# Kernel tuning notes

Hardware: AMD Instinct MI355X
Metric: run time of the kernel (lower is better)

The kernel has to match this reference:

```python
import jax, jax.numpy as jnp
import numpy as np

L, KV, H, D, DM, F, V = 6, 1, 4, 256, 1152, 6912, 65536
HIST, T = 4095, 1
EPS = 1e-6


def setup_inputs():
    key = jax.random.key(0)
    ks = jax.random.split(key, 24)
    n = lambda k, s, sc=0.02: jax.random.normal(k, s, dtype=jnp.float32) * sc
    sf = D ** -0.25  # head_dim^-0.25 baked into q/k norm weights as in the source
    return {
        "input_ids": jax.random.randint(ks[0], (1, T), 0, V, dtype=jnp.int32),
        "attn_flag": 0,  # decode step: additive causal mask zeroed, as in the repo
        "key_cache": n(ks[1], (L, KV, D, HIST), 0.5),
        "value_cache": n(ks[2], (L, KV, HIST, D), 0.5),
        "embed_table": jax.random.randint(ks[3], (V, DM), 0, 256, dtype=jnp.int32),
        "embed_scale": jax.random.uniform(ks[4], (V, 1), minval=1e-4, maxval=1e-2, dtype=jnp.float32),
        "embed_zp": -jax.random.uniform(ks[5], (V, 1), minval=0.0, maxval=0.5, dtype=jnp.float32),
        "w_in_ln": 1.0 + n(ks[6], (L, DM)),
        "w_q_norm": (1.0 + n(ks[7], (L, D))) * sf,
        "w_k_norm": (1.0 + n(ks[8], (L, D))) * sf,
        "Wq": n(ks[9], (L, DM, H * D)),
        "Wk": n(ks[10], (L, DM, KV * D)),
        "Wv": n(ks[11], (L, DM, KV * D)),
        "Wo": n(ks[12], (L, H * D, DM)),
        "w_post_attn_ln": 1.0 + n(ks[13], (L, DM)),
        "w_pre_ffn_ln": 1.0 + n(ks[14], (L, DM)),
        "w_post_ffn_ln": 1.0 + n(ks[15], (L, DM)),
        "Wg": n(ks[16], (L, DM, F)),
        "Wu": n(ks[17], (L, DM, F)),
        "Wd": n(ks[18], (L, F, DM)),
        "w_final_norm": 1.0 + n(ks[19], (DM,)),
        "W_lm": n(ks[20], (DM, V)),
        "is_sliding": (jnp.arange(L) % 6) != 5,  # 5 local : 1 global pattern
    }


def _rms(x, w):
    return w * x / jnp.sqrt(jnp.mean(x * x, axis=-1, keepdims=True) + EPS)


def _rot_half(x, axis):
    x1, x2 = jnp.split(x, 2, axis=axis)
    return jnp.concatenate([-x2, x1], axis=axis)


def _rope(base, hist, S, d):
    pos = jnp.arange(hist, S, dtype=jnp.float32)[:, None]
    theta = base ** (-(jnp.arange(0, d, 2, dtype=jnp.float32) / d))
    ang = pos * theta
    c = jnp.concatenate([jnp.cos(ang)] * 2, axis=-1).astype(jnp.float16).astype(jnp.float32)
    s = jnp.concatenate([jnp.sin(ang)] * 2, axis=-1).astype(jnp.float16).astype(jnp.float32)
    return c, s  # (T, D), half-precision roundtrip mimics the .half() tables


def reference(input_ids, attn_flag, key_cache, value_cache, embed_table, embed_scale,
              embed_zp, w_in_ln, w_q_norm, w_k_norm, Wq, Wk, Wv, Wo, w_post_attn_ln,
              w_pre_ffn_ln, w_post_ffn_ln, Wg, Wu, Wd, w_final_norm, W_lm, is_sliding):
    Lc, KVc, Dd, hist = key_cache.shape
    Tq = input_ids.shape[1]
    S = hist + Tq
    Hh = Wq.shape[-1] // Dd
    G = Hh // KVc
    cos_g, sin_g = _rope(10000.0, hist, S, Dd)    # assigned to 'global' exactly as in source
    cos_l, sin_l = _rope(1000000.0, hist, S, Dd)  # assigned to 'local'
    mask = (jnp.arange(S)[None, :] > jnp.arange(Tq)[:, None]).astype(jnp.float32) * (-128.0 * float(attn_flag))  # (T,S)
    # int8-dequant embedding lookup: uint8 codes * per-row scale + per-row zero point
    h = embed_table[input_ids].astype(jnp.float32) * embed_scale[input_ids] + embed_zp[input_ids]  # (1,T,DM)

    def body(h, xs):
        ck, cv, slide, w_in, w_qn, w_kn, wq, wk, wv, wo, w_pa, w_pf, w_pof, wg, wu, wd = xs
        cq = jnp.where(slide, cos_l, cos_g)
        sq = jnp.where(slide, sin_l, sin_g)
        ckk, skk = cq.T, sq.T  # (D,T) for keys
        resid = h
        hn = _rms(h, w_in)                                                  # (1,T,DM)
        q = _rms((hn @ wq).reshape(Tq, Hh, Dd), w_qn).transpose(1, 0, 2)    # (H,T,D)
        k = _rms((hn @ wk).reshape(Tq, KVc, Dd), w_kn).transpose(1, 2, 0)   # (KV,D,T)
        v = (hn @ wv).reshape(Tq, KVc, Dd).transpose(1, 0, 2)               # (KV,T,D)
        q = q * cq + _rot_half(q, -1) * sq
        k = k * ckk[None] + _rot_half(k, 1) * skk[None]
        kf = jnp.concatenate([ck, k], axis=-1)   # (KV,D,S) new key cache
        vf = jnp.concatenate([cv, v], axis=1)    # (KV,S,D) new value cache
        kr = jnp.repeat(kf, G, axis=0)           # GQA repeat -> (H,D,S)
        vr = jnp.repeat(vf, G, axis=0)           # (H,S,D)
        attn = jax.nn.softmax(jnp.einsum('htd,hds->hts', q, kr) + mask[None], axis=-1)
        ao = jnp.einsum('hts,hsd->htd', attn, vr).transpose(1, 0, 2).reshape(1, Tq, Hh * Dd) @ wo
        h = resid + _rms(ao, w_pa)
        resid = h
        x = _rms(h, w_pf)
        m = (jax.nn.gelu(x @ wg, approximate=True) * (x @ wu)) @ wd
        h = resid + _rms(m, w_pof)
        return h, (kf, vf)

    h, (keys, values) = jax.lax.scan(
        body, h,
        (key_cache, value_cache, is_sliding, w_in_ln, w_q_norm, w_k_norm, Wq, Wk, Wv, Wo,
         w_post_attn_ln, w_pre_ffn_ln, w_post_ffn_ln, Wg, Wu, Wd))
    last = _rms(h[:, -1], w_final_norm)          # (1,DM)
    logits = last @ W_lm                          # (1,V)
    token = jnp.argmax(logits, axis=-1, keepdims=True).astype(jnp.int32)
    return keys, values, token
```

## Files before the change

### kernel.cpp

```cpp
#include <hip/hip_runtime.h>
#include <hip/hip_fp16.h>
#include <cmath>

#define LNUM 6
#define DM   1152
#define DHEAD 256
#define NH   4
#define FF   6912
#define VOC  65536
#define HIST 4095
#define SEQ  4096
#define EPSV 1e-6f

__device__ __forceinline__ float block_sum(float v, float* red4) {
#pragma unroll
    for (int off = 32; off; off >>= 1) v += __shfl_xor(v, off);
    int t = threadIdx.x;
    if ((t & 63) == 0) red4[t >> 6] = v;
    __syncthreads();
    float r = red4[0] + red4[1] + red4[2] + red4[3];
    __syncthreads();
    return r;
}

__global__ __launch_bounds__(256) void gk_copy(const float* __restrict__ kc,
                                               const float* __restrict__ vc,
                                               float* __restrict__ keys,
                                               float* __restrict__ vals) {
    int b = blockIdx.x;
    if (b < 24576) {
        int row = b >> 4;
        int s = ((b & 15) << 8) + threadIdx.x;
        if (s < HIST) keys[(size_t)row * SEQ + s] = kc[(size_t)row * HIST + s];
    } else {
        int r = (b - 24576) * 4 + (threadIdx.x >> 6);
        int d4 = threadIdx.x & 63;
        if (r < LNUM * HIST) {
            int l = r / HIST, sI = r - l * HIST;
            ((float4*)(vals + ((size_t)l * SEQ + sI) * DHEAD))[d4] =
                ((const float4*)(vc + (size_t)r * DHEAD))[d4];
        }
    }
}

__global__ __launch_bounds__(256) void gk_qkv(
    const float* __restrict__ Wq, const float* __restrict__ Wk, const float* __restrict__ Wv,
    const float* __restrict__ w_in, const float* __restrict__ w_pof_prev,
    const float* __restrict__ hprev, const float* __restrict__ dprev,
    const int* __restrict__ ids, const int* __restrict__ tbl,
    const float* __restrict__ escale, const float* __restrict__ ezp,
    float* __restrict__ hin_out, float* __restrict__ qkv_out, int has_prev) {
    __shared__ float xv[DM];
    __shared__ float red4[4];
    int t = threadIdx.x;
    if (has_prev) {
        float ss = 0.f;
        for (int i = t; i < DM; i += 256) { float d = dprev[i]; ss += d * d; }
        ss = block_sum(ss, red4);
        float inv = 1.f / sqrtf(ss / DM + EPSV);
        for (int i = t; i < DM; i += 256)
            xv[i] = hprev[i] + w_pof_prev[i] * dprev[i] * inv;
    } else {
        int tok = ids[0];
        float sc = escale[tok], z = ezp[tok];
        const int* row = tbl + (size_t)tok * DM;
        for (int i = t; i < DM; i += 256) xv[i] = (float)row[i] * sc + z;
    }
    __syncthreads();
    if (blockIdx.x == 0 && blockIdx.y == 0)
        for (int i = t; i < DM; i += 256) hin_out[i] = xv[i];
    float ss = 0.f;
    for (int i = t; i < DM; i += 256) { float v = xv[i]; ss += v * v; }
    ss = block_sum(ss, red4);
    float inv = 1.f / sqrtf(ss / DM + EPSV);
    for (int i = t; i < DM; i += 256) xv[i] = w_in[i] * xv[i] * inv;
    __syncthreads();

    int j = blockIdx.x * 256 + t;
    const float* W; int jj, ncol;
    if (j < 1024)      { W = Wq; jj = j;        ncol = 1024; }
    else if (j < 1280) { W = Wk; jj = j - 1024; ncol = 256; }
    else               { W = Wv; jj = j - 1280; ncol = 256; }
    int i0 = blockIdx.y * 36;
    float acc = 0.f;
#pragma unroll 4
    for (int ii = 0; ii < 36; ++ii)
        acc += xv[i0 + ii] * W[(size_t)(i0 + ii) * ncol + jj];
    atomicAdd(&qkv_out[j], acc);
}

__global__ __launch_bounds__(256) void gk_attn(
    const float* __restrict__ qkv, const float* __restrict__ w_qn,
    const float* __restrict__ w_kn, const int* __restrict__ attn_flag,
    float* __restrict__ keys_l, float* __restrict__ vals_l,
    float* __restrict__ po_part, float* __restrict__ sum_part, float rope_base) {
    __shared__ float lq[NH * DHEAD];
    __shared__ float lqf[NH * DHEAD];
    __shared__ float lkn[DHEAD];
    __shared__ float lkf[DHEAD];
    __shared__ float lv[DHEAD];
    __shared__ float lp[NH * 32];
    __shared__ float red4[4];
    int t = threadIdx.x;
    int s0 = blockIdx.x * 32;
    bool last = (blockIdx.x == gridDim.x - 1);

    int jm = t & 127;
    float theta = powf(rope_base, -(float)(2 * jm) / 256.f);
    float ang = 4095.f * theta;
    float c = __half2float(__float2half(cosf(ang)));
    float s = __half2float(__float2half(sinf(ang)));

    for (int h = 0; h < NH; ++h) lq[h * 256 + t] = qkv[h * 256 + t];
    lkn[t] = qkv[1024 + t];
    lv[t]  = qkv[1280 + t];
    __syncthreads();
    for (int h = 0; h < NH; ++h) {
        float v = lq[h * 256 + t];
        float ss = block_sum(v * v, red4);
        float inv = 1.f / sqrtf(ss / 256.f + EPSV);
        float qn = w_qn[t] * v * inv;
        lq[h * 256 + t] = qn;
        __syncthreads();
        float partner = (t < 128) ? -lq[h * 256 + t + 128] : lq[h * 256 + t - 128];
        lqf[h * 256 + t] = qn * c + partner * s;
    }
    {
        float v = lkn[t];
        float ss = block_sum(v * v, red4);
        float inv = 1.f / sqrtf(ss / 256.f + EPSV);
        float kn = w_kn[t] * v * inv;
        lkn[t] = kn;
        __syncthreads();
        float partner = (t < 128) ? -lkn[t + 128] : lkn[t - 128];
        lkf[t] = kn * c + partner * s;
    }
    __syncthreads();
    if (last) {
        keys_l[(size_t)t * SEQ + (SEQ - 1)] = lkf[t];
        vals_l[(size_t)(SEQ - 1) * DHEAD + t] = lv[t];
    }
    int sl = t & 31, dc = t >> 5;
    int sg = s0 + sl;
    bool self = last && (sl == 31);
    float a0 = 0, a1 = 0, a2 = 0, a3 = 0;
#pragma unroll 4
    for (int dd = 0; dd < 32; ++dd) {
        int d = dc * 32 + dd;
        float kv = self ? lkf[d] : keys_l[(size_t)d * SEQ + sg];
        a0 += lqf[0 * 256 + d] * kv;
        a1 += lqf[1 * 256 + d] * kv;
        a2 += lqf[2 * 256 + d] * kv;
        a3 += lqf[3 * 256 + d] * kv;
    }
    __syncthreads();
    lq[0 * 256 + t] = a0; lq[1 * 256 + t] = a1; lq[2 * 256 + t] = a2; lq[3 * 256 + t] = a3;
    __syncthreads();
    if (t < 32) {
        int af = attn_flag[0];
        float mk = (s0 + t > 0) ? -128.f * (float)af : 0.f;
        for (int h = 0; h < NH; ++h) {
            float sc_ = 0.f;
#pragma unroll
            for (int d8 = 0; d8 < 8; ++d8) sc_ += lq[h * 256 + d8 * 32 + t];
            lp[h * 32 + t] = expf(sc_ + mk);
        }
    }
    __syncthreads();
    if (t < NH) {
        float su = 0.f;
        for (int i = 0; i < 32; ++i) su += lp[t * 32 + i];
        sum_part[blockIdx.x * NH + t] = su;
    }
    float p0 = 0, p1 = 0, p2 = 0, p3 = 0;
#pragma unroll 4
    for (int ss_ = 0; ss_ < 32; ++ss_) {
        float v = (last && ss_ == 31) ? lv[t] : vals_l[(size_t)(s0 + ss_) * DHEAD + t];
        p0 += lp[0 * 32 + ss_] * v;
        p1 += lp[1 * 32 + ss_] * v;
        p2 += lp[2 * 32 + ss_] * v;
        p3 += lp[3 * 32 + ss_] * v;
    }
    float* po = po_part + (size_t)blockIdx.x * NH * DHEAD;
    po[0 * 256 + t] = p0; po[1 * 256 + t] = p1; po[2 * 256 + t] = p2; po[3 * 256 + t] = p3;
}

__global__ __launch_bounds__(256) void gk_wo(
    const float* __restrict__ po_part, const float* __restrict__ sum_part,
    const float* __restrict__ Wo_l, float* __restrict__ aproj) {
    __shared__ float x[64];
    __shared__ float hinv[NH];
    __shared__ float red4[4];
    int t = threadIdx.x;
    for (int h = 0; h < NH; ++h) {
        float v = (t < 128) ? sum_part[t * NH + h] : 0.f;
        float tot = block_sum(v, red4);
        if (t == 0) hinv[h] = 1.f / tot;
    }
    __syncthreads();
    int i0 = blockIdx.y * 64;
    if (t < 64) {
        float a = 0.f;
#pragma unroll 8
        for (int b = 0; b < 128; ++b) a += po_part[(size_t)b * 1024 + i0 + t];
        x[t] = a * hinv[(i0 + t) >> 8];
    }
    __syncthreads();
    int j = blockIdx.x * 256 + t;
    if (j < DM) {
        float acc = 0.f;
#pragma unroll 4
        for (int ii = 0; ii < 64; ++ii)
            acc += x[ii] * Wo_l[(size_t)(i0 + ii) * DM + j];
        atomicAdd(&aproj[j], acc);
    }
}

__global__ __launch_bounds__(256) void gk_gu(
    const float* __restrict__ Wg_l, const float* __restrict__ Wu_l,
    const float* __restrict__ w_pa, const float* __restrict__ w_pf,
    const float* __restrict__ hin, const float* __restrict__ aproj,
    float* __restrict__ hmid_out, float* __restrict__ gup) {
    __shared__ float xv[DM];
    __shared__ float red4[4];
    int t = threadIdx.x;
    float ss = 0.f;
    for (int i = t; i < DM; i += 256) { float a = aproj[i]; ss += a * a; }
    ss = block_sum(ss, red4);
    float inv = 1.f / sqrtf(ss / DM + EPSV);
    for (int i = t; i < DM; i += 256) xv[i] = hin[i] + w_pa[i] * aproj[i] * inv;
    __syncthreads();
    if (blockIdx.x == 0 && blockIdx.y == 0)
        for (int i = t; i < DM; i += 256) hmid_out[i] = xv[i];
    float s2 = 0.f;
    for (int i = t; i < DM; i += 256) { float v = xv[i]; s2 += v * v; }
    s2 = block_sum(s2, red4);
    float inv2 = 1.f / sqrtf(s2 / DM + EPSV);
    for (int i = t; i < DM; i += 256) xv[i] = w_pf[i] * xv[i] * inv2;
    __syncthreads();

    int j2 = blockIdx.x * 256 + t;
    const float2* W2; int jj2; float* dst;
    if (j2 < FF / 2) { W2 = (const float2*)Wg_l; jj2 = j2;
                       dst = gup + (size_t)blockIdx.y * 2 * FF + 2 * j2; }
    else             { W2 = (const float2*)Wu_l; jj2 = j2 - FF / 2;
                       dst = gup + (size_t)blockIdx.y * 2 * FF + FF + 2 * (j2 - FF / 2); }
    int i0 = blockIdx.y * 72;
    float ax = 0.f, ay = 0.f;
#pragma unroll 4
    for (int ii = 0; ii < 72; ++ii) {
        float xs = xv[i0 + ii];
        float2 w = W2[(size_t)(i0 + ii) * (FF / 2) + jj2];
        ax += xs * w.x; ay += xs * w.y;
    }
    dst[0] = ax; dst[1] = ay;
}

__global__ __launch_bounds__(256) void gk_wd(const float* __restrict__ gup,
                                             const float* __restrict__ Wd_l,
                                             float* __restrict__ dproj) {
    __shared__ float m[108];
    int t = threadIdx.x;
    int i0 = blockIdx.y * 108;
    if (t < 108) {
        float g = 0.f, u = 0.f;
#pragma unroll
        for (int p = 0; p < 16; ++p) {
            g += gup[(size_t)p * 2 * FF + i0 + t];
            u += gup[(size_t)p * 2 * FF + FF + i0 + t];
        }
        float gl = 0.5f * g * (1.f + tanhf(0.7978845608028654f * (g + 0.044715f * g * g * g)));
        m[t] = gl * u;
    }
    __syncthreads();
    int j = blockIdx.x * 256 + t;
    if (j < DM) {
        float acc = 0.f;
#pragma unroll 4
        for (int ii = 0; ii < 108; ++ii)
            acc += m[ii] * Wd_l[(size_t)(i0 + ii) * DM + j];
        atomicAdd(&dproj[j], acc);
    }
}

__global__ __launch_bounds__(256) void gk_logits(
    const float* __restrict__ W_lm, const float* __restrict__ w_pof5,
    const float* __restrict__ w_fin, const float* __restrict__ hmid5,
    const float* __restrict__ dproj5, float* __restrict__ lgp) {
    __shared__ float xv[DM];
    __shared__ float red4[4];
    int t = threadIdx.x;
    float ss = 0.f;
    for (int i = t; i < DM; i += 256) { float d = dproj5[i]; ss += d * d; }
    ss = block_sum(ss, red4);
    float inv = 1.f / sqrtf(ss / DM + EPSV);
    for (int i = t; i < DM; i += 256) xv[i] = hmid5[i] + w_pof5[i] * dproj5[i] * inv;
    __syncthreads();
    float s2 = 0.f;
    for (int i = t; i < DM; i += 256) { float v = xv[i]; s2 += v * v; }
    s2 = block_sum(s2, red4);
    float inv2 = 1.f / sqrtf(s2 / DM + EPSV);
    for (int i = t; i < DM; i += 256) xv[i] = w_fin[i] * xv[i] * inv2;
    __syncthreads();

    int j2 = blockIdx.x * 256 + t;
    int i0 = blockIdx.y * 192;
    const float2* W2 = (const float2*)W_lm;
    float ax = 0.f, ay = 0.f;
#pragma unroll 4
    for (int ii = 0; ii < 192; ++ii) {
        float xs = xv[i0 + ii];
        float2 w = W2[(size_t)(i0 + ii) * (VOC / 2) + j2];
        ax += xs * w.x; ay += xs * w.y;
    }
    float* dst = lgp + (size_t)blockIdx.y * VOC + 2 * j2;
    dst[0] = ax; dst[1] = ay;
}

__global__ __launch_bounds__(256) void gk_amax1(const float* __restrict__ lgp,
                                                float* __restrict__ pv, float* __restrict__ pi) {
    __shared__ float rv[256];
    __shared__ int ri[256];
    int t = threadIdx.x;
    int c1 = blockIdx.x * 512 + t, c2 = c1 + 256;
    float v1 = 0.f, v2 = 0.f;
#pragma unroll
    for (int p = 0; p < 6; ++p) {
        v1 += lgp[(size_t)p * VOC + c1];
        v2 += lgp[(size_t)p * VOC + c2];
    }
    float bv; int bi;
    if (v1 >= v2) { bv = v1; bi = c1; } else { bv = v2; bi = c2; }
    rv[t] = bv; ri[t] = bi; __syncthreads();
    for (int off = 128; off > 0; off >>= 1) {
        if (t < off) {
            float ov = rv[t + off]; int oi = ri[t + off];
            if (ov > rv[t] || (ov == rv[t] && oi < ri[t])) { rv[t] = ov; ri[t] = oi; }
        }
        __syncthreads();
    }
    if (t == 0) { pv[blockIdx.x] = rv[0]; pi[blockIdx.x] = (float)ri[0]; }
}

__global__ __launch_bounds__(128) void gk_amax2(const float* __restrict__ pv,
                                                const float* __restrict__ pi,
                                                float* __restrict__ tok_out) {
    __shared__ float rv[128];
    __shared__ int ri[128];
    int t = threadIdx.x;
    rv[t] = pv[t]; ri[t] = (int)pi[t]; __syncthreads();
    for (int off = 64; off > 0; off >>= 1) {
        if (t < off) {
            float ov = rv[t + off]; int oi = ri[t + off];
            if (ov > rv[t] || (ov == rv[t] && oi < ri[t])) { rv[t] = ov; ri[t] = oi; }
        }
        __syncthreads();
    }
    if (t == 0) tok_out[0] = (float)ri[0];
}

extern "C" void kernel_launch(void* const* d_in, const int* in_sizes, int n_in,
                              void* d_out, int out_size, void* d_ws, size_t ws_size,
                              hipStream_t stream) {
    const int*   input_ids   = (const int*)d_in[0];
    const int*   attn_flag   = (const int*)d_in[1];
    const float* key_cache   = (const float*)d_in[2];
    const float* value_cache = (const float*)d_in[3];
    const int*   embed_table = (const int*)d_in[4];
    const float* embed_scale = (const float*)d_in[5];
    const float* embed_zp    = (const float*)d_in[6];
    const float* w_in_ln     = (const float*)d_in[7];
    const float* w_q_norm    = (const float*)d_in[8];
    const float* w_k_norm    = (const float*)d_in[9];
    const float* Wq          = (const float*)d_in[10];
    const float* Wk          = (const float*)d_in[11];
    const float* Wv          = (const float*)d_in[12];
    const float* Wo          = (const float*)d_in[13];
    const float* w_pa        = (const float*)d_in[14];
    const float* w_pf        = (const float*)d_in[15];
    const float* w_pof       = (const float*)d_in[16];
    const float* Wg          = (const float*)d_in[17];
    const float* Wu          = (const float*)d_in[18];
    const float* Wd          = (const float*)d_in[19];
    const float* w_fin       = (const float*)d_in[20];
    const float* W_lm        = (const float*)d_in[21];

    float* keys = (float*)d_out;
    float* vals = keys + (size_t)LNUM * DHEAD * SEQ;
    float* tok_out = vals + (size_t)LNUM * SEQ * DHEAD;

    float* ws = (float*)d_ws;
    const size_t QKV_O = 0;
    const size_t AP_O  = QKV_O + (size_t)LNUM * 1536;
    const size_t DP_O  = AP_O + (size_t)LNUM * DM;
    const size_t ZEND  = DP_O + (size_t)LNUM * DM;
    const size_t POP_O = ZEND;
    const size_t SPS_O = POP_O + 128 * 1024;
    const size_t GUP_O = SPS_O + 128 * NH;
    const size_t LGP_O = GUP_O + (size_t)16 * 2 * FF;
    const size_t HIN_O = LGP_O + (size_t)6 * VOC;
    const size_t HM_O  = HIN_O + (size_t)LNUM * DM;
    const size_t AMV_O = HM_O + (size_t)LNUM * DM;
    const size_t AMI_O = AMV_O + 128;

    hipMemsetAsync(ws, 0, ZEND * sizeof(float), stream);
    gk_copy<<<24576 + 6144, 256, 0, stream>>>(key_cache, value_cache, keys, vals);

    for (int l = 0; l < LNUM; ++l) {
        float* QKVl = ws + QKV_O + (size_t)l * 1536;
        float* APl  = ws + AP_O + (size_t)l * DM;
        float* DPl  = ws + DP_O + (size_t)l * DM;
        float* HINl = ws + HIN_O + (size_t)l * DM;
        float* HMl  = ws + HM_O + (size_t)l * DM;
        float* keys_l = keys + (size_t)l * DHEAD * SEQ;
        float* vals_l = vals + (size_t)l * SEQ * DHEAD;

        gk_qkv<<<dim3(6, 32), 256, 0, stream>>>(
            Wq + (size_t)l * DM * 1024, Wk + (size_t)l * DM * 256,
            Wv + (size_t)l * DM * 256, w_in_ln + (size_t)l * DM,
            w_pof + (size_t)(l ? l - 1 : 0) * DM,
            (l ? ws + HM_O + (size_t)(l - 1) * DM : nullptr),
            (l ? ws + DP_O + (size_t)(l - 1) * DM : nullptr),
            input_ids, embed_table, embed_scale, embed_zp,
            HINl, QKVl, (l > 0) ? 1 : 0);

        gk_attn<<<128, 256, 0, stream>>>(
            QKVl, w_q_norm + (size_t)l * DHEAD, w_k_norm + (size_t)l * DHEAD,
            attn_flag, keys_l, vals_l, ws + POP_O, ws + SPS_O,
            ((l % 6) != 5) ? 1000000.0f : 10000.0f);

        gk_wo<<<dim3(5, 16), 256, 0, stream>>>(
            ws + POP_O, ws + SPS_O, Wo + (size_t)l * 1024 * DM, APl);

        gk_gu<<<dim3(27, 16), 256, 0, stream>>>(
            Wg + (size_t)l * DM * FF, Wu + (size_t)l * DM * FF,
            w_pa + (size_t)l * DM, w_pf + (size_t)l * DM, HINl, APl, HMl, ws + GUP_O);

        gk_wd<<<dim3(5, 64), 256, 0, stream>>>(ws + GUP_O, Wd + (size_t)l * FF * DM, DPl);
    }

    gk_logits<<<dim3(128, 6), 256, 0, stream>>>(
        W_lm, w_pof + (size_t)5 * DM, w_fin,
        ws + HM_O + (size_t)5 * DM, ws + DP_O + (size_t)5 * DM, ws + LGP_O);
    gk_amax1<<<128, 256, 0, stream>>>(ws + LGP_O, ws + AMV_O, ws + AMI_O);
    gk_amax2<<<1, 128, 0, stream>>>(ws + AMV_O, ws + AMI_O, tok_out);
}
```

Baseline: 596.0 us.

## Restructure GEMV kernels to float4 loads with split-K in-block reduction and atomics

The QKV, gate/up, down and LM-head matrix-vector kernels now have each thread load 16 rows of float4 weights up front. A 4-way K split inside the block is reduced through shared memory, and the result is atomically accumulated into zeroed buffers. This replaces the partial-sum buffers and the reduction passes in gk_wd and amax1. The aim is wider memory transactions and more loads in flight, which helps these bandwidth-bound weight streams, and less partial-buffer traffic. The cost is more atomics, a larger memset region and extra register pressure from the 16 preloaded float4s.

```diff
diff --git a/kernel.cpp b/kernel.cpp
--- a/kernel.cpp
+++ b/kernel.cpp
@@ -12,7 +12,20 @@
 #define SEQ  4096
 #define EPSV 1e-6f
 
-__device__ __forceinline__ float block_sum(float v, float* red4) {
+#define QKV_O 0
+#define AP_O  9216
+#define DP_O  16128
+#define GU_O  23040
+#define LG_O  105984
+#define ZEND  171520
+#define POP_O 171520
+#define SPS_O 302592
+#define HIN_O 303104
+#define HM_O  310016
+#define AMV_O 316928
+#define AMI_O 317184
+
+__device__ __forceinline__ float block_sum256(float v, float* red4) {
 #pragma unroll
     for (int off = 32; off; off >>= 1) v += __shfl_xor(v, off);
     int t = threadIdx.x;
@@ -52,11 +65,12 @@
     float* __restrict__ hin_out, float* __restrict__ qkv_out, int has_prev) {
     __shared__ float xv[DM];
     __shared__ float red4[4];
+    __shared__ float4 qred[256];
     int t = threadIdx.x;
     if (has_prev) {
         float ss = 0.f;
         for (int i = t; i < DM; i += 256) { float d = dprev[i]; ss += d * d; }
-        ss = block_sum(ss, red4);
+        ss = block_sum256(ss, red4);
         float inv = 1.f / sqrtf(ss / DM + EPSV);
         for (int i = t; i < DM; i += 256)
             xv[i] = hprev[i] + w_pof_prev[i] * dprev[i] * inv;
@@ -71,22 +85,37 @@
         for (int i = t; i < DM; i += 256) hin_out[i] = xv[i];
     float ss = 0.f;
     for (int i = t; i < DM; i += 256) { float v = xv[i]; ss += v * v; }
-    ss = block_sum(ss, red4);
+    ss = block_sum256(ss, red4);
     float inv = 1.f / sqrtf(ss / DM + EPSV);
     for (int i = t; i < DM; i += 256) xv[i] = w_in[i] * xv[i] * inv;
     __syncthreads();
 
-    int j = blockIdx.x * 256 + t;
-    const float* W; int jj, ncol;
-    if (j < 1024)      { W = Wq; jj = j;        ncol = 1024; }
-    else if (j < 1280) { W = Wk; jj = j - 1024; ncol = 256; }
-    else               { W = Wv; jj = j - 1280; ncol = 256; }
-    int i0 = blockIdx.y * 36;
-    float acc = 0.f;
-#pragma unroll 4
-    for (int ii = 0; ii < 36; ++ii)
-        acc += xv[i0 + ii] * W[(size_t)(i0 + ii) * ncol + jj];
-    atomicAdd(&qkv_out[j], acc);
+    int f4c = t & 63, ks = t >> 6;
+    int jf = blockIdx.x * 64 + f4c;
+    const float4* W4; int jj4, ncol4;
+    if (jf < 256)      { W4 = (const float4*)Wq; jj4 = jf;       ncol4 = 256; }
+    else if (jf < 320) { W4 = (const float4*)Wk; jj4 = jf - 256; ncol4 = 64; }
+    else               { W4 = (const float4*)Wv; jj4 = jf - 320; ncol4 = 64; }
+    int i0 = blockIdx.y * 64 + ks * 16;
+    float4 w[16];
+#pragma unroll
+    for (int r = 0; r < 16; ++r) w[r] = W4[(size_t)(i0 + r) * ncol4 + jj4];
+    float4 acc = {0, 0, 0, 0};
+#pragma unroll
+    for (int r = 0; r < 16; ++r) {
+        float xs = xv[i0 + r];
+        acc.x += xs * w[r].x; acc.y += xs * w[r].y;
+        acc.z += xs * w[r].z; acc.w += xs * w[r].w;
+    }
+    qred[t] = acc;
+    __syncthreads();
+    if (ks == 0) {
+        float4 a = qred[f4c], b = qred[64 + f4c], c = qred[128 + f4c], d = qred[192 + f4c];
+        atomicAdd(&qkv_out[4 * jf + 0], a.x + b.x + c.x + d.x);
+        atomicAdd(&qkv_out[4 * jf + 1], a.y + b.y + c.y + d.y);
+        atomicAdd(&qkv_out[4 * jf + 2], a.z + b.z + c.z + d.z);
+        atomicAdd(&qkv_out[4 * jf + 3], a.w + b.w + c.w + d.w);
+    }
 }
 
 __global__ __launch_bounds__(256) void gk_attn(
@@ -117,7 +146,7 @@
     __syncthreads();
     for (int h = 0; h < NH; ++h) {
         float v = lq[h * 256 + t];
-        float ss = block_sum(v * v, red4);
+        float ss = block_sum256(v * v, red4);
         float inv = 1.f / sqrtf(ss / 256.f + EPSV);
         float qn = w_qn[t] * v * inv;
         lq[h * 256 + t] = qn;
@@ -127,7 +156,7 @@
     }
     {
         float v = lkn[t];
-        float ss = block_sum(v * v, red4);
+        float ss = block_sum256(v * v, red4);
         float inv = 1.f / sqrtf(ss / 256.f + EPSV);
         float kn = w_kn[t] * v * inv;
         lkn[t] = kn;
@@ -194,7 +223,7 @@
     int t = threadIdx.x;
     for (int h = 0; h < NH; ++h) {
         float v = (t < 128) ? sum_part[t * NH + h] : 0.f;
-        float tot = block_sum(v, red4);
+        float tot = block_sum256(v, red4);
         if (t == 0) hinv[h] = 1.f / tot;
     }
     __syncthreads();
@@ -220,13 +249,14 @@
     const float* __restrict__ Wg_l, const float* __restrict__ Wu_l,
     const float* __restrict__ w_pa, const float* __restrict__ w_pf,
     const float* __restrict__ hin, const float* __restrict__ aproj,
-    float* __restrict__ hmid_out, float* __restrict__ gup) {
+    float* __restrict__ hmid_out, float* __restrict__ gu_out) {
     __shared__ float xv[DM];
     __shared__ float red4[4];
+    __shared__ float4 gred[256];
     int t = threadIdx.x;
     float ss = 0.f;
     for (int i = t; i < DM; i += 256) { float a = aproj[i]; ss += a * a; }
-    ss = block_sum(ss, red4);
+    ss = block_sum256(ss, red4);
     float inv = 1.f / sqrtf(ss / DM + EPSV);
     for (int i = t; i < DM; i += 256) xv[i] = hin[i] + w_pa[i] * aproj[i] * inv;
     __syncthreads();
@@ -234,104 +264,133 @@
         for (int i = t; i < DM; i += 256) hmid_out[i] = xv[i];
     float s2 = 0.f;
     for (int i = t; i < DM; i += 256) { float v = xv[i]; s2 += v * v; }
-    s2 = block_sum(s2, red4);
+    s2 = block_sum256(s2, red4);
     float inv2 = 1.f / sqrtf(s2 / DM + EPSV);
     for (int i = t; i < DM; i += 256) xv[i] = w_pf[i] * xv[i] * inv2;
     __syncthreads();
 
-    int j2 = blockIdx.x * 256 + t;
-    const float2* W2; int jj2; float* dst;
-    if (j2 < FF / 2) { W2 = (const float2*)Wg_l; jj2 = j2;
-                       dst = gup + (size_t)blockIdx.y * 2 * FF + 2 * j2; }
-    else             { W2 = (const float2*)Wu_l; jj2 = j2 - FF / 2;
-                       dst = gup + (size_t)blockIdx.y * 2 * FF + FF + 2 * (j2 - FF / 2); }
-    int i0 = blockIdx.y * 72;
-    float ax = 0.f, ay = 0.f;
-#pragma unroll 4
-    for (int ii = 0; ii < 72; ++ii) {
-        float xs = xv[i0 + ii];
-        float2 w = W2[(size_t)(i0 + ii) * (FF / 2) + jj2];
-        ax += xs * w.x; ay += xs * w.y;
-    }
-    dst[0] = ax; dst[1] = ay;
-}
-
-__global__ __launch_bounds__(256) void gk_wd(const float* __restrict__ gup,
+    int f4c = t & 63, ks = t >> 6;
+    int cgi = blockIdx.x;
+    bool isU = cgi >= 27;
+    int cg = isU ? cgi - 27 : cgi;
+    const float4* W4 = (const float4*)(isU ? Wu_l : Wg_l);
+    int colf4 = cg * 64 + f4c;
+    int i0 = blockIdx.y * 64 + ks * 16;
+    float4 w[16];
+#pragma unroll
+    for (int r = 0; r < 16; ++r) w[r] = W4[(size_t)(i0 + r) * 1728 + colf4];
+    float4 acc = {0, 0, 0, 0};
+#pragma unroll
+    for (int r = 0; r < 16; ++r) {
+        float xs = xv[i0 + r];
+        acc.x += xs * w[r].x; acc.y += xs * w[r].y;
+        acc.z += xs * w[r].z; acc.w += xs * w[r].w;
+    }
+    gred[t] = acc;
+    __syncthreads();
+    if (ks == 0) {
+        float4 a = gred[f4c], b = gred[64 + f4c], c = gred[128 + f4c], d = gred[192 + f4c];
+        float* dst = gu_out + (isU ? FF : 0) + 4 * colf4;
+        atomicAdd(dst + 0, a.x + b.x + c.x + d.x);
+        atomicAdd(dst + 1, a.y + b.y + c.y + d.y);
+        atomicAdd(dst + 2, a.z + b.z + c.z + d.z);
+        atomicAdd(dst + 3, a.w + b.w + c.w + d.w);
+    }
+}
+
+__global__ __launch_bounds__(256) void gk_wd(const float* __restrict__ gu,
                                              const float* __restrict__ Wd_l,
                                              float* __restrict__ dproj) {
-    __shared__ float m[108];
-    int t = threadIdx.x;
-    int i0 = blockIdx.y * 108;
-    if (t < 108) {
-        float g = 0.f, u = 0.f;
-#pragma unroll
-        for (int p = 0; p < 16; ++p) {
-            g += gup[(size_t)p * 2 * FF + i0 + t];
-            u += gup[(size_t)p * 2 * FF + FF + i0 + t];
-        }
+    __shared__ float m[64];
+    __shared__ float4 wred[256];
+    int t = threadIdx.x;
+    int i0 = blockIdx.y * 64;
+    if (t < 64) {
+        float g = gu[i0 + t], u = gu[FF + i0 + t];
         float gl = 0.5f * g * (1.f + tanhf(0.7978845608028654f * (g + 0.044715f * g * g * g)));
         m[t] = gl * u;
     }
     __syncthreads();
-    int j = blockIdx.x * 256 + t;
-    if (j < DM) {
-        float acc = 0.f;
-#pragma unroll 4
-        for (int ii = 0; ii < 108; ++ii)
-            acc += m[ii] * Wd_l[(size_t)(i0 + ii) * DM + j];
-        atomicAdd(&dproj[j], acc);
+    int f4c = t & 63, ks = t >> 6;
+    int col4 = blockIdx.x * 64 + f4c;
+    float4 acc = {0, 0, 0, 0};
+    if (col4 < 288) {
+        const float4* W4 = (const float4*)Wd_l;
+        float4 w[16];
+#pragma unroll
+        for (int r = 0; r < 16; ++r) w[r] = W4[(size_t)(i0 + ks * 16 + r) * 288 + col4];
+#pragma unroll
+        for (int r = 0; r < 16; ++r) {
+            float xs = m[ks * 16 + r];
+            acc.x += xs * w[r].x; acc.y += xs * w[r].y;
+            acc.z += xs * w[r].z; acc.w += xs * w[r].w;
+        }
+    }
+    wred[t] = acc;
+    __syncthreads();
+    if (ks == 0 && col4 < 288) {
+        float4 a = wred[f4c], b = wred[64 + f4c], c = wred[128 + f4c], d = wred[192 + f4c];
+        atomicAdd(&dproj[4 * col4 + 0], a.x + b.x + c.x + d.x);
+        atomicAdd(&dproj[4 * col4 + 1], a.y + b.y + c.y + d.y);
+        atomicAdd(&dproj[4 * col4 + 2], a.z + b.z + c.z + d.z);
+        atomicAdd(&dproj[4 * col4 + 3], a.w + b.w + c.w + d.w);
     }
 }
 
 __global__ __launch_bounds__(256) void gk_logits(
     const float* __restrict__ W_lm, const float* __restrict__ w_pof5,
     const float* __restrict__ w_fin, const float* __restrict__ hmid5,
-    const float* __restrict__ dproj5, float* __restrict__ lgp) {
+    const float* __restrict__ dproj5, float* __restrict__ lg) {
     __shared__ float xv[DM];
     __shared__ float red4[4];
+    __shared__ float4 lred[256];
     int t = threadIdx.x;
     float ss = 0.f;
     for (int i = t; i < DM; i += 256) { float d = dproj5[i]; ss += d * d; }
-    ss = block_sum(ss, red4);
+    ss = block_sum256(ss, red4);
     float inv = 1.f / sqrtf(ss / DM + EPSV);
     for (int i = t; i < DM; i += 256) xv[i] = hmid5[i] + w_pof5[i] * dproj5[i] * inv;
     __syncthreads();
     float s2 = 0.f;
     for (int i = t; i < DM; i += 256) { float v = xv[i]; s2 += v * v; }
-    s2 = block_sum(s2, red4);
+    s2 = block_sum256(s2, red4);
     float inv2 = 1.f / sqrtf(s2 / DM + EPSV);
     for (int i = t; i < DM; i += 256) xv[i] = w_fin[i] * xv[i] * inv2;
     __syncthreads();
 
-    int j2 = blockIdx.x * 256 + t;
-    int i0 = blockIdx.y * 192;
-    const float2* W2 = (const float2*)W_lm;
-    float ax = 0.f, ay = 0.f;
-#pragma unroll 4
-    for (int ii = 0; ii < 192; ++ii) {
-        float xs = xv[i0 + ii];
-        float2 w = W2[(size_t)(i0 + ii) * (VOC / 2) + j2];
-        ax += xs * w.x; ay += xs * w.y;
-    }
-    float* dst = lgp + (size_t)blockIdx.y * VOC + 2 * j2;
-    dst[0] = ax; dst[1] = ay;
-}
-
-__global__ __launch_bounds__(256) void gk_amax1(const float* __restrict__ lgp,
+    int f4c = t & 63, ks = t >> 6;
+    int colf4 = blockIdx.x * 64 + f4c;
+    int i0 = blockIdx.y * 64 + ks * 16;
+    const float4* W4 = (const float4*)W_lm;
+    float4 w[16];
+#pragma unroll
+    for (int r = 0; r < 16; ++r) w[r] = W4[(size_t)(i0 + r) * 16384 + colf4];
+    float4 acc = {0, 0, 0, 0};
+#pragma unroll
+    for (int r = 0; r < 16; ++r) {
+        float xs = xv[i0 + r];
+        acc.x += xs * w[r].x; acc.y += xs * w[r].y;
+        acc.z += xs * w[r].z; acc.w += xs * w[r].w;
+    }
+    lred[t] = acc;
+    __syncthreads();
+    if (ks == 0) {
+        float4 a = lred[f4c], b = lred[64 + f4c], c = lred[128 + f4c], d = lred[192 + f4c];
+        atomicAdd(&lg[4 * colf4 + 0], a.x + b.x + c.x + d.x);
+        atomicAdd(&lg[4 * colf4 + 1], a.y + b.y + c.y + d.y);
+        atomicAdd(&lg[4 * colf4 + 2], a.z + b.z + c.z + d.z);
+        atomicAdd(&lg[4 * colf4 + 3], a.w + b.w + c.w + d.w);
+    }
+}
+
+__global__ __launch_bounds__(256) void gk_amax1(const float* __restrict__ lg,
                                                 float* __restrict__ pv, float* __restrict__ pi) {
     __shared__ float rv[256];
     __shared__ int ri[256];
     int t = threadIdx.x;
-    int c1 = blockIdx.x * 512 + t, c2 = c1 + 256;
-    float v1 = 0.f, v2 = 0.f;
-#pragma unroll
-    for (int p = 0; p < 6; ++p) {
-        v1 += lgp[(size_t)p * VOC + c1];
-        v2 += lgp[(size_t)p * VOC + c2];
-    }
-    float bv; int bi;
-    if (v1 >= v2) { bv = v1; bi = c1; } else { bv = v2; bi = c2; }
-    rv[t] = bv; ri[t] = bi; __syncthreads();
+    int c = blockIdx.x * 256 + t;
+    rv[t] = lg[c]; ri[t] = c;
+    __syncthreads();
     for (int off = 128; off > 0; off >>= 1) {
         if (t < off) {
             float ov = rv[t + off]; int oi = ri[t + off];
@@ -342,14 +401,15 @@
     if (t == 0) { pv[blockIdx.x] = rv[0]; pi[blockIdx.x] = (float)ri[0]; }
 }
 
-__global__ __launch_bounds__(128) void gk_amax2(const float* __restrict__ pv,
+__global__ __launch_bounds__(256) void gk_amax2(const float* __restrict__ pv,
                                                 const float* __restrict__ pi,
                                                 float* __restrict__ tok_out) {
-    __shared__ float rv[128];
-    __shared__ int ri[128];
-    int t = threadIdx.x;
-    rv[t] = pv[t]; ri[t] = (int)pi[t]; __syncthreads();
-    for (int off = 64; off > 0; off >>= 1) {
+    __shared__ float rv[256];
+    __shared__ int ri[256];
+    int t = threadIdx.x;
+    rv[t] = pv[t]; ri[t] = (int)pi[t];
+    __syncthreads();
+    for (int off = 128; off > 0; off >>= 1) {
         if (t < off) {
             float ov = rv[t + off]; int oi = ri[t + off];
             if (ov > rv[t] || (ov == rv[t] && oi < ri[t])) { rv[t] = ov; ri[t] = oi; }
@@ -362,86 +422,73 @@
 extern "C" void kernel_launch(void* const* d_in, const int* in_sizes, int n_in,
                               void* d_out, int out_size, void* d_ws, size_t ws_size,
                               hipStream_t stream) {
-    const int*   input_ids   = (const int*)d_in[0];
-    const int*   attn_flag   = (const int*)d_in[1];
-    const float* key_cache   = (const float*)d_in[2];
-    const float* value_cache = (const float*)d_in[3];
-    const int*   embed_table = (const int*)d_in[4];
-    const float* embed_scale = (const float*)d_in[5];
-    const float* embed_zp    = (const float*)d_in[6];
-    const float* w_in_ln     = (const float*)d_in[7];
-    const float* w_q_norm    = (const float*)d_in[8];
-    const float* w_k_norm    = (const float*)d_in[9];
-    const float* Wq          = (const float*)d_in[10];
-    const float* Wk          = (const float*)d_in[11];
-    const float* Wv          = (const float*)d_in[12];
-    const float* Wo          = (const float*)d_in[13];
-    const float* w_pa        = (const float*)d_in[14];
-    const float* w_pf        = (const float*)d_in[15];
-    const float* w_pof       = (const float*)d_in[16];
-    const float* Wg          = (const float*)d_in[17];
-    const float* Wu          = (const float*)d_in[18];
-    const float* Wd          = (const float*)d_in[19];
-    const float* w_fin       = (const float*)d_in[20];
-    const float* W_lm        = (const float*)d_in[21];
+    const int*   ids   = (const int*)d_in[0];
+    const int*   aflag = (const int*)d_in[1];
+    const float* kc    = (const float*)d_in[2];
+    const float* vc    = (const float*)d_in[3];
+    const int*   tbl   = (const int*)d_in[4];
+    const float* esc   = (const float*)d_in[5];
+    const float* ezp   = (const float*)d_in[6];
+    const float* w_in  = (const float*)d_in[7];
+    const float* w_qn  = (const float*)d_in[8];
+    const float* w_kn  = (const float*)d_in[9];
+    const float* Wq    = (const float*)d_in[10];
+    const float* Wk    = (const float*)d_in[11];
+    const float* Wv    = (const float*)d_in[12];
+    const float* Wo    = (const float*)d_in[13];
+    const float* w_pa  = (const float*)d_in[14];
+    const float* w_pf  = (const float*)d_in[15];
+    const float* w_pof = (const float*)d_in[16];
+    const float* Wg    = (const float*)d_in[17];
+    const float* Wu    = (const float*)d_in[18];
+    const float* Wd    = (const float*)d_in[19];
+    const float* w_fin = (const float*)d_in[20];
+    const float* Wlm   = (const float*)d_in[21];
 
     float* keys = (float*)d_out;
     float* vals = keys + (size_t)LNUM * DHEAD * SEQ;
-    float* tok_out = vals + (size_t)LNUM * SEQ * DHEAD;
-
+    float* tok  = vals + (size_t)LNUM * SEQ * DHEAD;
     float* ws = (float*)d_ws;
-    const size_t QKV_O = 0;
-    const size_t AP_O  = QKV_O + (size_t)LNUM * 1536;
-    const size_t DP_O  = AP_O + (size_t)LNUM * DM;
-    const size_t ZEND  = DP_O + (size_t)LNUM * DM;
-    const size_t POP_O = ZEND;
-    const size_t SPS_O = POP_O + 128 * 1024;
-    const size_t GUP_O = SPS_O + 128 * NH;
-    const size_t LGP_O = GUP_O + (size_t)16 * 2 * FF;
-    const size_t HIN_O = LGP_O + (size_t)6 * VOC;
-    const size_t HM_O  = HIN_O + (size_t)LNUM * DM;
-    const size_t AMV_O = HM_O + (size_t)LNUM * DM;
-    const size_t AMI_O = AMV_O + 128;
 
     hipMemsetAsync(ws, 0, ZEND * sizeof(float), stream);
-    gk_copy<<<24576 + 6144, 256, 0, stream>>>(key_cache, value_cache, keys, vals);
+    gk_copy<<<24576 + 6144, 256, 0, stream>>>(kc, vc, keys, vals);
 
     for (int l = 0; l < LNUM; ++l) {
         float* QKVl = ws + QKV_O + (size_t)l * 1536;
         float* APl  = ws + AP_O + (size_t)l * DM;
         float* DPl  = ws + DP_O + (size_t)l * DM;
+        float* GUl  = ws + GU_O + (size_t)l * 2 * FF;
         float* HINl = ws + HIN_O + (size_t)l * DM;
         float* HMl  = ws + HM_O + (size_t)l * DM;
         float* keys_l = keys + (size_t)l * DHEAD * SEQ;
         float* vals_l = vals + (size_t)l * SEQ * DHEAD;
 
-        gk_qkv<<<dim3(6, 32), 256, 0, stream>>>(
+        gk_qkv<<<dim3(6, 18), 256, 0, stream>>>(
             Wq + (size_t)l * DM * 1024, Wk + (size_t)l * DM * 256,
-            Wv + (size_t)l * DM * 256, w_in_ln + (size_t)l * DM,
+            Wv + (size_t)l * DM * 256, w_in + (size_t)l * DM,
             w_pof + (size_t)(l ? l - 1 : 0) * DM,
             (l ? ws + HM_O + (size_t)(l - 1) * DM : nullptr),
             (l ? ws + DP_O + (size_t)(l - 1) * DM : nullptr),
-            input_ids, embed_table, embed_scale, embed_zp,
-            HINl, QKVl, (l > 0) ? 1 : 0);
+            ids, tbl, esc, ezp, HINl, QKVl, (l > 0) ? 1 : 0);
 
         gk_attn<<<128, 256, 0, stream>>>(
-            QKVl, w_q_norm + (size_t)l * DHEAD, w_k_norm + (size_t)l * DHEAD,
-            attn_flag, keys_l, vals_l, ws + POP_O, ws + SPS_O,
+            QKVl, w_qn + (size_t)l * DHEAD, w_kn + (size_t)l * DHEAD,
+            aflag, keys_l, vals_l, ws + POP_O, ws + SPS_O,
             ((l % 6) != 5) ? 1000000.0f : 10000.0f);
 
         gk_wo<<<dim3(5, 16), 256, 0, stream>>>(
             ws + POP_O, ws + SPS_O, Wo + (size_t)l * 1024 * DM, APl);
 
-        gk_gu<<<dim3(27, 16), 256, 0, stream>>>(
+        gk_gu<<<dim3(54, 18), 256, 0, stream>>>(
             Wg + (size_t)l * DM * FF, Wu + (size_t)l * DM * FF,
-            w_pa + (size_t)l * DM, w_pf + (size_t)l * DM, HINl, APl, HMl, ws + GUP_O);
-
-        gk_wd<<<dim3(5, 64), 256, 0, stream>>>(ws + GUP_O, Wd + (size_t)l * FF * DM, DPl);
-    }
-
-    gk_logits<<<dim3(128, 6), 256, 0, stream>>>(
-        W_lm, w_pof + (size_t)5 * DM, w_fin,
-        ws + HM_O + (size_t)5 * DM, ws + DP_O + (size_t)5 * DM, ws + LGP_O);
-    gk_amax1<<<128, 256, 0, stream>>>(ws + LGP_O, ws + AMV_O, ws + AMI_O);
-    gk_amax2<<<1, 128, 0, stream>>>(ws + AMV_O, ws + AMI_O, tok_out);
-}
+            w_pa + (size_t)l * DM, w_pf + (size_t)l * DM, HINl, APl, HMl, GUl);
+
+        gk_wd<<<dim3(5, 108), 256, 0, stream>>>(GUl, Wd + (size_t)l * FF * DM, DPl);
+    }
+
+    gk_logits<<<dim3(256, 18), 256, 0, stream>>>(
+        Wlm, w_pof + (size_t)5 * DM, w_fin,
+        ws + HM_O + (size_t)5 * DM, ws + DP_O + (size_t)5 * DM, ws + LG_O);
+    gk_amax1<<<256, 256, 0, stream>>>(ws + LG_O, ws + AMV_O, ws + AMI_O);
+    gk_amax2<<<1, 256, 0, stream>>>(ws + AMV_O, ws + AMI_O, tok);
+}
```

After: 579.1 us. -2.8%, faster.
